# Performance work log

Hardware: AMD Instinct MI355X
Metric: run time of the kernel (lower is better)

The kernel has to match this reference:

```python
import jax, jax.numpy as jnp
import numpy as np

N_NODES = 100000
N_EDGES = 1600000
IN_CH = 128
HID = 128
OUT_CH = 16
N_GRAPHS = 64


def setup_inputs() -> dict:
    key = jax.random.key(0)
    ks = jax.random.split(key, 8)
    x = jax.random.normal(ks[0], (N_NODES, IN_CH), dtype=jnp.float32)
    edge_index = jax.random.randint(ks[1], (2, N_EDGES), 0, N_NODES, dtype=jnp.int64)
    batch = jnp.sort(jax.random.randint(ks[2], (N_NODES,), 0, N_GRAPHS, dtype=jnp.int64))
    s1 = 1.0 / np.sqrt(IN_CH)
    s2 = 1.0 / np.sqrt(HID)
    W1 = jax.random.uniform(ks[3], (IN_CH, HID), jnp.float32, -s1, s1)
    b1 = jnp.zeros((HID,), jnp.float32)
    W2 = jax.random.uniform(ks[4], (HID, HID), jnp.float32, -s2, s2)
    b2 = jnp.zeros((HID,), jnp.float32)
    Wfc = jax.random.uniform(ks[5], (HID, OUT_CH), jnp.float32, -s2, s2)
    bfc = jax.random.uniform(ks[6], (OUT_CH,), jnp.float32, -s2, s2)
    return {"x": x, "W1": W1, "b1": b1, "W2": W2, "b2": b2,
            "Wfc": Wfc, "bfc": bfc, "edge_index": edge_index, "batch": batch}


def _gcn_conv(x, W, b, src, dst, deg_inv_sqrt, deg_inv):
    # GCNConv with self-loops: out = D^-1/2 (A+I) D^-1/2 (x W) + b
    h = x @ W                                   # [N, H]
    norm = deg_inv_sqrt[src] * deg_inv_sqrt[dst]  # [E]
    agg = jax.ops.segment_sum(h[src] * norm[:, None], dst, num_segments=N_NODES)
    # self-loop term: deg_inv_sqrt[i]^2 * h[i]
    return agg + h * deg_inv[:, None] + b


def reference(x, W1, b1, W2, b2, Wfc, bfc, edge_index, batch):
    src, dst = edge_index[0], edge_index[1]
    # degree including self-loop
    deg = jax.ops.segment_sum(jnp.ones((N_EDGES,), jnp.float32), dst, num_segments=N_NODES) + 1.0
    deg_inv_sqrt = jax.lax.rsqrt(deg)
    deg_inv = 1.0 / deg
    h = jax.nn.relu(_gcn_conv(x, W1, b1, src, dst, deg_inv_sqrt, deg_inv))
    h = jax.nn.relu(_gcn_conv(h, W2, b2, src, dst, deg_inv_sqrt, deg_inv))
    # global mean pool over graphs
    sums = jax.ops.segment_sum(h, batch, num_segments=N_GRAPHS)          # [G, H]
    counts = jax.ops.segment_sum(jnp.ones((N_NODES,), jnp.float32), batch, num_segments=N_GRAPHS)
    pooled = sums / jnp.maximum(counts, 1.0)[:, None]
    return pooled @ Wfc + bfc
```

## Files before the change

kernel.cpp:

```cpp
#include <hip/hip_runtime.h>
#include <math.h>

#define NN 100000
#define NE 1600000
#define CH 128
#define OUTC 16
#define NG 64

#define CBSH 9
#define NCB 196
#define CHK 8192
#define MAXB 12288
#define PS 8

typedef __attribute__((ext_vector_type(8))) short bf16x8;
typedef __attribute__((ext_vector_type(4))) float f32x4;

__device__ __forceinline__ unsigned short f2bf(float f) {
    union { float f; unsigned u; } v; v.f = f;
    unsigned r = v.u + 0x7FFF + ((v.u >> 16) & 1);
    return (unsigned short)(r >> 16);
}
__device__ __forceinline__ float bflo(unsigned u) {
    union { unsigned u; float f; } v; v.u = u << 16; return v.f;
}
__device__ __forceinline__ float bfhi(unsigned u) {
    union { unsigned u; float f; } v; v.u = u & 0xffff0000u; return v.f;
}

__global__ void k_prep(const float* __restrict__ W1, const float* __restrict__ W2,
                       unsigned short* __restrict__ wt1, unsigned short* __restrict__ wt2,
                       const int* __restrict__ batch, int* __restrict__ gptr,
                       int* __restrict__ bcnt) {
    int i = blockIdx.x * 256 + threadIdx.x;
    if (i < CH * CH) {
        int k = i >> 7, n = i & 127;
        wt1[n * CH + k] = f2bf(W1[i]);
    } else if (i < 2 * CH * CH) {
        int j = i - CH * CH;
        int k = j >> 7, n = j & 127;
        wt2[n * CH + k] = f2bf(W2[j]);
    }
    if (i < NCB) bcnt[i] = 0;
    if (i < NN) {
        int b = batch[i];
        int prev = (i == 0) ? -1 : batch[i - 1];
        for (int g = prev + 1; g <= b; g++) gptr[g] = i;
        if (i == NN - 1) {
            for (int g = b + 1; g <= NG; g++) gptr[g] = NN;
        }
    }
}

__global__ __launch_bounds__(1024) void k_hist(const int* __restrict__ dst, int* __restrict__ bcnt) {
    __shared__ int h[NCB];
    int t = threadIdx.x;
    if (t < NCB) h[t] = 0;
    __syncthreads();
    int base = blockIdx.x * CHK;
#pragma unroll
    for (int i = 0; i < 8; i++) {
        int e = base + i * 1024 + t;
        if (e < NE) atomicAdd(&h[dst[e] >> CBSH], 1);
    }
    __syncthreads();
    if (t < NCB && h[t]) atomicAdd(&bcnt[t], h[t]);
}

__global__ __launch_bounds__(1024) void k_bscan(const int* __restrict__ bcnt, int* __restrict__ ebase,
                        int* __restrict__ gfill, float* __restrict__ pooled) {
    __shared__ int s[256];
    int t = threadIdx.x;
    if (t < 256) s[t] = (t < NCB) ? bcnt[t] : 0;
    __syncthreads();
    for (int off = 1; off < 256; off <<= 1) {
        int v = 0;
        if (t < 256 && t >= off) v = s[t - off];
        __syncthreads();
        if (t < 256) s[t] += v;
        __syncthreads();
    }
    if (t == 0) ebase[0] = 0;
    if (t < NCB) { ebase[t + 1] = s[t]; gfill[t] = 0; }
    for (int i = t; i < NG * CH; i += 1024) pooled[i] = 0.f;
}

__global__ __launch_bounds__(1024) void k_passA(const int* __restrict__ src, const int* __restrict__ dst,
                        const int* __restrict__ ebase, int* __restrict__ gfill,
                        unsigned* __restrict__ ebuf) {
    __shared__ unsigned lbuf[CHK];
    __shared__ unsigned char lbyte[CHK];
    __shared__ int hcnt[NCB];
    __shared__ int hbase[256];
    __shared__ int goff[NCB];
    int t = threadIdx.x;
    if (t < NCB) hcnt[t] = 0;
    __syncthreads();
    int base = blockIdx.x * CHK;
    int cb[8], slot[8]; unsigned pk[8];
#pragma unroll
    for (int i = 0; i < 8; i++) {
        int e = base + i * 1024 + t;
        cb[i] = -1;
        if (e < NE) {
            int d = dst[e], s = src[e];
            cb[i] = d >> CBSH;
            pk[i] = ((unsigned)s << CBSH) | (unsigned)(d & 511);
            slot[i] = atomicAdd(&hcnt[cb[i]], 1);
        }
    }
    __syncthreads();
    if (t < 256) hbase[t] = (t < NCB) ? hcnt[t] : 0;
    __syncthreads();
    for (int off = 1; off < 256; off <<= 1) {
        int v = 0;
        if (t < 256 && t >= off) v = hbase[t - off];
        __syncthreads();
        if (t < 256) hbase[t] += v;
        __syncthreads();
    }
    if (t < NCB) {
        int c = hcnt[t];
        int g = c ? atomicAdd(&gfill[t], c) : 0;
        goff[t] = ebase[t] + g - (hbase[t] - c);
    }
    __syncthreads();
#pragma unroll
    for (int i = 0; i < 8; i++) {
        if (cb[i] >= 0) {
            int pos = hbase[cb[i]] - hcnt[cb[i]] + slot[i];
            lbuf[pos] = pk[i];
            lbyte[pos] = (unsigned char)cb[i];
        }
    }
    __syncthreads();
    int total = min(NE - base, CHK);
    for (int p = t; p < total; p += 1024) {
        unsigned v = lbuf[p];
        int b = lbyte[p];
        ebuf[goff[b] + p] = v;
    }
}

__global__ __launch_bounds__(1024) void k_passB(const unsigned* __restrict__ ebuf, const int* __restrict__ ebase,
                        int* __restrict__ degi, int* __restrict__ rowst,
                        float* __restrict__ dis, int* __restrict__ csr) {
    __shared__ int cnt[512];
    __shared__ int nbase[512];
    __shared__ int fill[512];
    __shared__ int stage[MAXB];
    int t = threadIdx.x;
    int cb = blockIdx.x;
    int nb0 = cb << CBSH;
    int ncnt = min(512, NN - nb0);
    int e0 = ebase[cb], e1 = ebase[cb + 1];
    if (t < 512) { cnt[t] = 0; fill[t] = 0; }
    __syncthreads();
    for (int e = e0 + t; e < e1; e += 1024)
        atomicAdd(&cnt[ebuf[e] & 511], 1);
    __syncthreads();
    if (t < 512) nbase[t] = cnt[t];
    __syncthreads();
    for (int off = 1; off < 512; off <<= 1) {
        int v = 0;
        if (t < 512 && t >= off) v = nbase[t - off];
        __syncthreads();
        if (t < 512) nbase[t] += v;
        __syncthreads();
    }
    for (int e = e0 + t; e < e1; e += 1024) {
        unsigned v = ebuf[e];
        int local = v & 511;
        int s = atomicAdd(&fill[local], 1);
        stage[nbase[local] - cnt[local] + s] = (int)(v >> CBSH);
    }
    __syncthreads();
    int total = e1 - e0;
    for (int p = t; p < total; p += 1024) csr[e0 + p] = stage[p];
    if (t < ncnt) {
        int c = cnt[t];
        degi[nb0 + t] = c;
        rowst[nb0 + t] = e0 + nbase[t] - c;
        dis[nb0 + t] = rsqrtf((float)c + 1.0f);
    }
}

template<bool F32IN>
__launch_bounds__(256, 2)
__global__ void k_gemm(const void* __restrict__ Av,
                       const unsigned short* __restrict__ WT,
                       const float* __restrict__ dis,
                       unsigned short* __restrict__ out) {
    int tid = threadIdx.x;
    int wave = tid >> 6, lane = tid & 63;
    int quad = lane >> 4, l16 = lane & 15;

    int rbase = blockIdx.x * 128 + wave * 32;

    bf16x8 af[2][4];
#pragma unroll
    for (int s = 0; s < 2; s++) {
        int row = rbase + s * 16 + l16;
        if (row >= NN) row = NN - 1;
        if (F32IN) {
            const float* arow = (const float*)Av + (size_t)row * CH + quad * 8;
#pragma unroll
            for (int ks = 0; ks < 4; ks++) {
                float4 lo = *(const float4*)(arow + ks * 32);
                float4 hi = *(const float4*)(arow + ks * 32 + 4);
                union { bf16x8 v; unsigned short u[8]; } tmp;
                tmp.u[0] = f2bf(lo.x); tmp.u[1] = f2bf(lo.y);
                tmp.u[2] = f2bf(lo.z); tmp.u[3] = f2bf(lo.w);
                tmp.u[4] = f2bf(hi.x); tmp.u[5] = f2bf(hi.y);
                tmp.u[6] = f2bf(hi.z); tmp.u[7] = f2bf(hi.w);
                af[s][ks] = tmp.v;
            }
        } else {
            const unsigned short* arow = (const unsigned short*)Av + (size_t)row * CH + quad * 8;
#pragma unroll
            for (int ks = 0; ks < 4; ks++) af[s][ks] = *(const bf16x8*)(arow + ks * 32);
        }
    }

    f32x4 acc[2][8];
#pragma unroll
    for (int s = 0; s < 2; s++)
#pragma unroll
        for (int t = 0; t < 8; t++) acc[s][t] = (f32x4){0.f, 0.f, 0.f, 0.f};

#pragma unroll
    for (int t = 0; t < 8; t++) {
        const unsigned short* wcol = WT + (size_t)(t * 16 + l16) * CH + quad * 8;
        bf16x8 b0 = *(const bf16x8*)(wcol);
        bf16x8 b1 = *(const bf16x8*)(wcol + 32);
        bf16x8 b2 = *(const bf16x8*)(wcol + 64);
        bf16x8 b3 = *(const bf16x8*)(wcol + 96);
#pragma unroll
        for (int s = 0; s < 2; s++) {
            acc[s][t] = __builtin_amdgcn_mfma_f32_16x16x32_bf16(af[s][0], b0, acc[s][t], 0, 0, 0);
            acc[s][t] = __builtin_amdgcn_mfma_f32_16x16x32_bf16(af[s][1], b1, acc[s][t], 0, 0, 0);
            acc[s][t] = __builtin_amdgcn_mfma_f32_16x16x32_bf16(af[s][2], b2, acc[s][t], 0, 0, 0);
            acc[s][t] = __builtin_amdgcn_mfma_f32_16x16x32_bf16(af[s][3], b3, acc[s][t], 0, 0, 0);
        }
    }

#pragma unroll
    for (int s = 0; s < 2; s++) {
#pragma unroll
        for (int r = 0; r < 4; r++) {
            int orow = rbase + s * 16 + quad * 4 + r;
            if (orow < NN) {
                float d = dis[orow];
#pragma unroll
                for (int t = 0; t < 8; t++) {
                    out[(size_t)orow * CH + t * 16 + l16] = f2bf(acc[s][t][r] * d);
                }
            }
        }
    }
}

__global__ __launch_bounds__(256) void k_agg(const unsigned short* __restrict__ ht, const int* __restrict__ rowst,
                      const int* __restrict__ degi, const int* __restrict__ csr,
                      const float* __restrict__ dis, const float* __restrict__ bias,
                      unsigned short* __restrict__ out) {
    int t = threadIdx.x;
    int grp = t >> 4;
    int q = t & 15;
    int n = blockIdx.x * 16 + grp;
    const uint4* base = (const uint4*)ht;

    uint4 sv = base[(size_t)n * 16 + q];
    float a[8];
    a[0] = bflo(sv.x); a[1] = bfhi(sv.x);
    a[2] = bflo(sv.y); a[3] = bfhi(sv.y);
    a[4] = bflo(sv.z); a[5] = bfhi(sv.z);
    a[6] = bflo(sv.w); a[7] = bfhi(sv.w);

    int start = rowst[n];
    int c = degi[n];
    int nb = c & ~7;
    int j = 0;
    for (; j < nb; j += 8) {
        int idx[8];
#pragma unroll
        for (int u = 0; u < 8; u++) idx[u] = csr[start + j + u];
        uint4 v[8];
#pragma unroll
        for (int u = 0; u < 8; u++) v[u] = base[(size_t)idx[u] * 16 + q];
#pragma unroll
        for (int u = 0; u < 8; u++) {
            a[0] += bflo(v[u].x); a[1] += bfhi(v[u].x);
            a[2] += bflo(v[u].y); a[3] += bfhi(v[u].y);
            a[4] += bflo(v[u].z); a[5] += bfhi(v[u].z);
            a[6] += bflo(v[u].w); a[7] += bfhi(v[u].w);
        }
    }
    if (j < c) {
        int idx[8];
#pragma unroll
        for (int u = 0; u < 8; u++) { int e = j + u; idx[u] = csr[start + (e < c ? e : c - 1)]; }
        uint4 v[8];
#pragma unroll
        for (int u = 0; u < 8; u++) v[u] = base[(size_t)idx[u] * 16 + q];
#pragma unroll
        for (int u = 0; u < 8; u++) {
            if (j + u < c) {
                a[0] += bflo(v[u].x); a[1] += bfhi(v[u].x);
                a[2] += bflo(v[u].y); a[3] += bfhi(v[u].y);
                a[4] += bflo(v[u].z); a[5] += bfhi(v[u].z);
                a[6] += bflo(v[u].w); a[7] += bfhi(v[u].w);
            }
        }
    }

    float d = dis[n];
    const float4* bp = (const float4*)bias;
    float4 b0 = bp[q * 2], b1 = bp[q * 2 + 1];
    uint4 o;
    {
        float ox = fmaxf(fmaf(d, a[0], b0.x), 0.f), oy = fmaxf(fmaf(d, a[1], b0.y), 0.f);
        o.x = ((unsigned)f2bf(oy) << 16) | (unsigned)f2bf(ox);
        ox = fmaxf(fmaf(d, a[2], b0.z), 0.f); oy = fmaxf(fmaf(d, a[3], b0.w), 0.f);
        o.y = ((unsigned)f2bf(oy) << 16) | (unsigned)f2bf(ox);
        ox = fmaxf(fmaf(d, a[4], b1.x), 0.f); oy = fmaxf(fmaf(d, a[5], b1.y), 0.f);
        o.z = ((unsigned)f2bf(oy) << 16) | (unsigned)f2bf(ox);
        ox = fmaxf(fmaf(d, a[6], b1.z), 0.f); oy = fmaxf(fmaf(d, a[7], b1.w), 0.f);
        o.w = ((unsigned)f2bf(oy) << 16) | (unsigned)f2bf(ox);
    }
    ((uint4*)out)[(size_t)n * 16 + q] = o;
}

__global__ __launch_bounds__(512) void k_pool2(const unsigned short* __restrict__ h,
                                               const int* __restrict__ gptr,
                                               float* __restrict__ pooled) {
    int g = blockIdx.x >> 3;
    int s = blockIdx.x & 7;
    int gs = gptr[g], ge = gptr[g + 1];
    int len = ge - gs;
    int i0 = gs + (int)(((long long)len * s) >> 3);
    int i1 = gs + (int)(((long long)len * (s + 1)) >> 3);
    int t = threadIdx.x;
    int pr = t & 63;
    int ro = t >> 6;
    const unsigned* base = (const unsigned*)h;
    float s0 = 0.f, s1 = 0.f;
    for (int n = i0 + ro; n < i1; n += 8) {
        unsigned v = base[(size_t)n * 64 + pr];
        s0 += bflo(v); s1 += bfhi(v);
    }
    __shared__ float red[2][8][64];
    red[0][ro][pr] = s0; red[1][ro][pr] = s1;
    __syncthreads();
    for (int off = 4; off >= 1; off >>= 1) {
        if (ro < off) {
            red[0][ro][pr] += red[0][ro + off][pr];
            red[1][ro][pr] += red[1][ro + off][pr];
        }
        __syncthreads();
    }
    if (ro == 0) {
        atomicAdd(&pooled[g * CH + pr * 2],     red[0][0][pr]);
        atomicAdd(&pooled[g * CH + pr * 2 + 1], red[1][0][pr]);
    }
}

__global__ void k_final(const float* __restrict__ pooled, const int* __restrict__ gptr,
                        const float* __restrict__ Wfc, const float* __restrict__ bfc,
                        float* __restrict__ out) {
    int idx = blockIdx.x * 256 + threadIdx.x;
    if (idx >= NG * OUTC) return;
    int g = idx >> 4, o = idx & 15;
    float c = (float)(gptr[g + 1] - gptr[g]);
    float inv = 1.0f / fmaxf(c, 1.0f);
    float s = 0.f;
    for (int k = 0; k < CH; k++) s += pooled[g * CH + k] * Wfc[k * OUTC + o];
    out[idx] = fmaf(s, inv, bfc[o]);
}

extern "C" void kernel_launch(void* const* d_in, const int* in_sizes, int n_in,
                              void* d_out, int out_size, void* d_ws, size_t ws_size,
                              hipStream_t stream) {
    (void)in_sizes; (void)n_in; (void)out_size; (void)ws_size;
    const float* x   = (const float*)d_in[0];
    const float* W1  = (const float*)d_in[1];
    const float* b1  = (const float*)d_in[2];
    const float* W2  = (const float*)d_in[3];
    const float* b2  = (const float*)d_in[4];
    const float* Wfc = (const float*)d_in[5];
    const float* bfc = (const float*)d_in[6];
    const int* ei    = (const int*)d_in[7];
    const int* batch = (const int*)d_in[8];
    const int* esrc = ei;
    const int* edst = ei + NE;
    float* out = (float*)d_out;

    char* w = (char*)d_ws;
    unsigned short* bufA = (unsigned short*)w; w += (size_t)NN * CH * 2;
    unsigned short* bufB = (unsigned short*)w; w += (size_t)NN * CH * 2;
    unsigned short* wt1  = (unsigned short*)w; w += (size_t)CH * CH * 2;
    unsigned short* wt2  = (unsigned short*)w; w += (size_t)CH * CH * 2;
    unsigned* ebuf = (unsigned*)w; w += (size_t)NE * 4;
    int* csr    = (int*)w;    w += (size_t)NE * 4;
    int* degi   = (int*)w;    w += (size_t)NN * 4;
    int* rowst  = (int*)w;    w += (size_t)NN * 4;
    float* dis  = (float*)w;  w += (size_t)NN * 4;
    int* bcnt   = (int*)w;    w += NCB * 4;
    int* ebase  = (int*)w;    w += (NCB + 1) * 4;
    int* gfill  = (int*)w;    w += NCB * 4;
    int* gptr   = (int*)w;    w += (NG + 1) * 4;
    float* pooled = (float*)w; w += (size_t)NG * CH * 4;

    const int histBlocks = (NE + CHK - 1) / CHK;
    const int gemmBlocks = (NN + 127) / 128;
    const int aggBlocks  = NN / 16;

    k_prep<<<(NN + 255) / 256, 256, 0, stream>>>(W1, W2, wt1, wt2, batch, gptr, bcnt);
    k_hist<<<histBlocks, 1024, 0, stream>>>(edst, bcnt);
    k_bscan<<<1, 1024, 0, stream>>>(bcnt, ebase, gfill, pooled);
    k_passA<<<histBlocks, 1024, 0, stream>>>(esrc, edst, ebase, gfill, ebuf);
    k_passB<<<NCB, 1024, 0, stream>>>(ebuf, ebase, degi, rowst, dis, csr);

    k_gemm<true><<<gemmBlocks, 256, 0, stream>>>(x, wt1, dis, bufA);
    k_agg<<<aggBlocks, 256, 0, stream>>>(bufA, rowst, degi, csr, dis, b1, bufB);
    k_gemm<false><<<gemmBlocks, 256, 0, stream>>>(bufB, wt2, dis, bufA);
    k_agg<<<aggBlocks, 256, 0, stream>>>(bufA, rowst, degi, csr, dis, b2, bufB);

    k_pool2<<<NG * PS, 512, 0, stream>>>(bufB, gptr, pooled);
    k_final<<<(NG * OUTC + 255) / 256, 256, 0, stream>>>(pooled, gptr, Wfc, bfc, out);
}
```

Before: 319.2 us.

## Slice feature tables into 16-channel column blocks for cache-local neighbor gathers

Stores the hidden feature matrices as 8 column slices of 16 bf16 channels (slice-major), and splits aggregation so each block handles one slice for 128 nodes. Each slice table (~3.2MB) is meant to fit in cache, so random neighbor gathers hit L2/LLC instead of DRAM. Neighbor indices for the block are staged in LDS, and degree is derived from rowst[n+1] instead of a separate array. The cost is that every edge index is re-read once per slice (8x), and each gather fetches only 32 bytes, down from 256.

Measured after the change: 338.3 us. +6.0%, slower.

```diff
diff --git a/kernel.cpp b/kernel.cpp
--- a/kernel.cpp
+++ b/kernel.cpp
@@ -12,6 +12,8 @@
 #define CHK 8192
 #define MAXB 12288
 #define PS 8
+#define ANB 128
+#define ICAP 3072
 
 typedef __attribute__((ext_vector_type(8))) short bf16x8;
 typedef __attribute__((ext_vector_type(4))) float f32x4;
@@ -27,6 +29,7 @@
 __device__ __forceinline__ float bfhi(unsigned u) {
     union { unsigned u; float f; } v; v.u = u & 0xffff0000u; return v.f;
 }
+
 
 __global__ void k_prep(const float* __restrict__ W1, const float* __restrict__ W2,
                        unsigned short* __restrict__ wt1, unsigned short* __restrict__ wt2,
@@ -143,7 +146,7 @@
 }
 
 __global__ __launch_bounds__(1024) void k_passB(const unsigned* __restrict__ ebuf, const int* __restrict__ ebase,
-                        int* __restrict__ degi, int* __restrict__ rowst,
+                        int* __restrict__ rowst,
                         float* __restrict__ dis, int* __restrict__ csr) {
     __shared__ int cnt[512];
     __shared__ int nbase[512];
@@ -179,10 +182,10 @@
     for (int p = t; p < total; p += 1024) csr[e0 + p] = stage[p];
     if (t < ncnt) {
         int c = cnt[t];
-        degi[nb0 + t] = c;
         rowst[nb0 + t] = e0 + nbase[t] - c;
         dis[nb0 + t] = rsqrtf((float)c + 1.0f);
     }
+    if (cb == NCB - 1 && t == 0) rowst[NN] = e1;
 }
 
 template<bool F32IN>
@@ -216,9 +219,13 @@
                 af[s][ks] = tmp.v;
             }
         } else {
-            const unsigned short* arow = (const unsigned short*)Av + (size_t)row * CH + quad * 8;
-#pragma unroll
-            for (int ks = 0; ks < 4; ks++) af[s][ks] = *(const bf16x8*)(arow + ks * 32);
+            const unsigned short* A = (const unsigned short*)Av;
+#pragma unroll
+            for (int ks = 0; ks < 4; ks++) {
+                int c = ks * 32 + quad * 8;
+                const unsigned short* p = A + ((size_t)(c >> 4) * NN + row) * 16 + (c & 15);
+                af[s][ks] = *(const bf16x8*)p;
+            }
         }
     }
 
@@ -253,72 +260,91 @@
                 float d = dis[orow];
 #pragma unroll
                 for (int t = 0; t < 8; t++) {
-                    out[(size_t)orow * CH + t * 16 + l16] = f2bf(acc[s][t][r] * d);
+                    out[((size_t)t * NN + orow) * 16 + l16] = f2bf(acc[s][t][r] * d);
                 }
             }
         }
     }
 }
 
-__global__ __launch_bounds__(256) void k_agg(const unsigned short* __restrict__ ht, const int* __restrict__ rowst,
-                      const int* __restrict__ degi, const int* __restrict__ csr,
-                      const float* __restrict__ dis, const float* __restrict__ bias,
+__global__ __launch_bounds__(256) void k_agg(const unsigned short* __restrict__ ht,
+                      const int* __restrict__ rowst,
+                      const float* __restrict__ dis, const int* __restrict__ csr,
+                      const float* __restrict__ bias,
                       unsigned short* __restrict__ out) {
-    int t = threadIdx.x;
-    int grp = t >> 4;
-    int q = t & 15;
-    int n = blockIdx.x * 16 + grp;
-    const uint4* base = (const uint4*)ht;
-
-    uint4 sv = base[(size_t)n * 16 + q];
-    float a[8];
-    a[0] = bflo(sv.x); a[1] = bfhi(sv.x);
-    a[2] = bflo(sv.y); a[3] = bfhi(sv.y);
-    a[4] = bflo(sv.z); a[5] = bfhi(sv.z);
-    a[6] = bflo(sv.w); a[7] = bfhi(sv.w);
-
-    int start = rowst[n];
-    int c = degi[n];
-    int nb = c & ~7;
-    int j = 0;
-    for (; j < nb; j += 8) {
-        int idx[8];
-#pragma unroll
-        for (int u = 0; u < 8; u++) idx[u] = csr[start + j + u];
-        uint4 v[8];
-#pragma unroll
-        for (int u = 0; u < 8; u++) v[u] = base[(size_t)idx[u] * 16 + q];
-#pragma unroll
-        for (int u = 0; u < 8; u++) {
-            a[0] += bflo(v[u].x); a[1] += bfhi(v[u].x);
-            a[2] += bflo(v[u].y); a[3] += bfhi(v[u].y);
-            a[4] += bflo(v[u].z); a[5] += bfhi(v[u].z);
-            a[6] += bflo(v[u].w); a[7] += bfhi(v[u].w);
-        }
-    }
-    if (j < c) {
-        int idx[8];
-#pragma unroll
-        for (int u = 0; u < 8; u++) { int e = j + u; idx[u] = csr[start + (e < c ? e : c - 1)]; }
-        uint4 v[8];
-#pragma unroll
-        for (int u = 0; u < 8; u++) v[u] = base[(size_t)idx[u] * 16 + q];
-#pragma unroll
-        for (int u = 0; u < 8; u++) {
-            if (j + u < c) {
-                a[0] += bflo(v[u].x); a[1] += bfhi(v[u].x);
-                a[2] += bflo(v[u].y); a[3] += bfhi(v[u].y);
-                a[4] += bflo(v[u].z); a[5] += bfhi(v[u].z);
-                a[6] += bflo(v[u].w); a[7] += bfhi(v[u].w);
+    __shared__ int sidx[ICAP];
+    int t = threadIdx.x;
+    int sl = blockIdx.x & 7;
+    int g0 = (blockIdx.x >> 3) * ANB;
+    int p = t & 1;
+    int n = g0 + (t >> 1);
+    const uint4* tab = (const uint4*)(ht + (size_t)sl * NN * 16);
+
+    int start = 0, c = 0; float d = 0.f; uint4 sv = (uint4){0u,0u,0u,0u};
+    if (n < NN) {
+        start = rowst[n];
+        c = rowst[n + 1] - start;
+        d = dis[n];
+        sv = tab[(size_t)n * 2 + p];
+    }
+
+    int nlast = min(g0 + ANB - 1, NN - 1);
+    int s0 = rowst[g0];
+    int len = rowst[nlast + 1] - s0;
+    bool fast = (len <= ICAP);
+    if (fast) {
+        for (int i = t; i < len; i += 256) sidx[i] = csr[s0 + i];
+    }
+    __syncthreads();
+
+    if (n < NN) {
+        float a[8];
+        a[0] = bflo(sv.x); a[1] = bfhi(sv.x);
+        a[2] = bflo(sv.y); a[3] = bfhi(sv.y);
+        a[4] = bflo(sv.z); a[5] = bfhi(sv.z);
+        a[6] = bflo(sv.w); a[7] = bfhi(sv.w);
+
+        int off = start - s0;
+        if (fast) {
+            for (int j = 0; j < c; j += 8) {
+                int idx[8];
+#pragma unroll
+                for (int u = 0; u < 8; u++) { int e = j + u; idx[u] = sidx[off + (e < c ? e : c - 1)]; }
+                uint4 v[8];
+#pragma unroll
+                for (int u = 0; u < 8; u++) v[u] = tab[(size_t)idx[u] * 2 + p];
+#pragma unroll
+                for (int u = 0; u < 8; u++) {
+                    if (j + u >= c) v[u] = (uint4){0u, 0u, 0u, 0u};
+                    a[0] += bflo(v[u].x); a[1] += bfhi(v[u].x);
+                    a[2] += bflo(v[u].y); a[3] += bfhi(v[u].y);
+                    a[4] += bflo(v[u].z); a[5] += bfhi(v[u].z);
+                    a[6] += bflo(v[u].w); a[7] += bfhi(v[u].w);
+                }
             }
-        }
-    }
-
-    float d = dis[n];
-    const float4* bp = (const float4*)bias;
-    float4 b0 = bp[q * 2], b1 = bp[q * 2 + 1];
-    uint4 o;
-    {
+        } else {
+            for (int j = 0; j < c; j += 8) {
+                int idx[8];
+#pragma unroll
+                for (int u = 0; u < 8; u++) { int e = j + u; idx[u] = csr[start + (e < c ? e : c - 1)]; }
+                uint4 v[8];
+#pragma unroll
+                for (int u = 0; u < 8; u++) v[u] = tab[(size_t)idx[u] * 2 + p];
+#pragma unroll
+                for (int u = 0; u < 8; u++) {
+                    if (j + u >= c) v[u] = (uint4){0u, 0u, 0u, 0u};
+                    a[0] += bflo(v[u].x); a[1] += bfhi(v[u].x);
+                    a[2] += bflo(v[u].y); a[3] += bfhi(v[u].y);
+                    a[4] += bflo(v[u].z); a[5] += bfhi(v[u].z);
+                    a[6] += bflo(v[u].w); a[7] += bfhi(v[u].w);
+                }
+            }
+        }
+
+        const float* bb = bias + sl * 16 + p * 8;
+        float4 b0 = *(const float4*)bb;
+        float4 b1 = *(const float4*)(bb + 4);
+        uint4 o;
         float ox = fmaxf(fmaf(d, a[0], b0.x), 0.f), oy = fmaxf(fmaf(d, a[1], b0.y), 0.f);
         o.x = ((unsigned)f2bf(oy) << 16) | (unsigned)f2bf(ox);
         ox = fmaxf(fmaf(d, a[2], b0.z), 0.f); oy = fmaxf(fmaf(d, a[3], b0.w), 0.f);
@@ -327,8 +353,8 @@
         o.z = ((unsigned)f2bf(oy) << 16) | (unsigned)f2bf(ox);
         ox = fmaxf(fmaf(d, a[6], b1.z), 0.f); oy = fmaxf(fmaf(d, a[7], b1.w), 0.f);
         o.w = ((unsigned)f2bf(oy) << 16) | (unsigned)f2bf(ox);
-    }
-    ((uint4*)out)[(size_t)n * 16 + q] = o;
+        ((uint4*)out)[((size_t)sl * NN + n) * 2 + p] = o;
+    }
 }
 
 __global__ __launch_bounds__(512) void k_pool2(const unsigned short* __restrict__ h,
@@ -343,10 +369,11 @@
     int t = threadIdx.x;
     int pr = t & 63;
     int ro = t >> 6;
+    int sl = pr >> 3, wd = pr & 7;
     const unsigned* base = (const unsigned*)h;
     float s0 = 0.f, s1 = 0.f;
     for (int n = i0 + ro; n < i1; n += 8) {
-        unsigned v = base[(size_t)n * 64 + pr];
+        unsigned v = base[((size_t)sl * NN + n) * 8 + wd];
         s0 += bflo(v); s1 += bfhi(v);
     }
     __shared__ float red[2][8][64];
@@ -402,8 +429,7 @@
     unsigned short* wt2  = (unsigned short*)w; w += (size_t)CH * CH * 2;
     unsigned* ebuf = (unsigned*)w; w += (size_t)NE * 4;
     int* csr    = (int*)w;    w += (size_t)NE * 4;
-    int* degi   = (int*)w;    w += (size_t)NN * 4;
-    int* rowst  = (int*)w;    w += (size_t)NN * 4;
+    int* rowst  = (int*)w;    w += (size_t)(NN + 1) * 4;
     float* dis  = (float*)w;  w += (size_t)NN * 4;
     int* bcnt   = (int*)w;    w += NCB * 4;
     int* ebase  = (int*)w;    w += (NCB + 1) * 4;
@@ -413,18 +439,18 @@
 
     const int histBlocks = (NE + CHK - 1) / CHK;
     const int gemmBlocks = (NN + 127) / 128;
-    const int aggBlocks  = NN / 16;
+    const int aggBlocks  = ((NN + ANB - 1) / ANB) * 8;
 
     k_prep<<<(NN + 255) / 256, 256, 0, stream>>>(W1, W2, wt1, wt2, batch, gptr, bcnt);
     k_hist<<<histBlocks, 1024, 0, stream>>>(edst, bcnt);
     k_bscan<<<1, 1024, 0, stream>>>(bcnt, ebase, gfill, pooled);
     k_passA<<<histBlocks, 1024, 0, stream>>>(esrc, edst, ebase, gfill, ebuf);
-    k_passB<<<NCB, 1024, 0, stream>>>(ebuf, ebase, degi, rowst, dis, csr);
+    k_passB<<<NCB, 1024, 0, stream>>>(ebuf, ebase, rowst, dis, csr);
 
     k_gemm<true><<<gemmBlocks, 256, 0, stream>>>(x, wt1, dis, bufA);
-    k_agg<<<aggBlocks, 256, 0, stream>>>(bufA, rowst, degi, csr, dis, b1, bufB);
+    k_agg<<<aggBlocks, 256, 0, stream>>>(bufA, rowst, dis, csr, b1, bufB);
     k_gemm<false><<<gemmBlocks, 256, 0, stream>>>(bufB, wt2, dis, bufA);
-    k_agg<<<aggBlocks, 256, 0, stream>>>(bufA, rowst, degi, csr, dis, b2, bufB);
+    k_agg<<<aggBlocks, 256, 0, stream>>>(bufA, rowst, dis, csr, b2, bufB);
 
     k_pool2<<<NG * PS, 512, 0, stream>>>(bufB, gptr, pooled);
     k_final<<<(NG * OUTC + 255) / 256, 256, 0, stream>>>(pooled, gptr, Wfc, bfc, out);
```

## Fold bucket scan into consumers, fuse pool with final FC, vectorize GEMM stores

Applied to the files above, without the earlier changes.

Removes the single-block bucket-scan kernel: passA and passB each recompute the prefix sum of bucket counts in shared memory, and the zeroing of gfill and pooled moves into k_prep. The pooling kernel now also does the final FC, using a done counter so the last block to finish computes the output, which removes one more launch. The GEMM swaps its MFMA operands so each lane holds four consecutive columns of one row and writes them as a packed 8-byte store instead of scattered 2-byte stores. Together this saves two kernel launches at the cost of redundant scans in every block and a serialized final FC in one block.

New measurement: 332.9 us. 4.3% more time.

```diff
diff --git a/kernel.cpp b/kernel.cpp
--- a/kernel.cpp
+++ b/kernel.cpp
@@ -31,7 +31,8 @@
 __global__ void k_prep(const float* __restrict__ W1, const float* __restrict__ W2,
                        unsigned short* __restrict__ wt1, unsigned short* __restrict__ wt2,
                        const int* __restrict__ batch, int* __restrict__ gptr,
-                       int* __restrict__ bcnt) {
+                       int* __restrict__ bcnt, int* __restrict__ gfill,
+                       float* __restrict__ pooled, int* __restrict__ done) {
     int i = blockIdx.x * 256 + threadIdx.x;
     if (i < CH * CH) {
         int k = i >> 7, n = i & 127;
@@ -41,7 +42,9 @@
         int k = j >> 7, n = j & 127;
         wt2[n * CH + k] = f2bf(W2[j]);
     }
-    if (i < NCB) bcnt[i] = 0;
+    if (i < NCB) { bcnt[i] = 0; gfill[i] = 0; }
+    if (i < NG * CH) pooled[i] = 0.f;
+    if (i == 0) *done = 0;
     if (i < NN) {
         int b = batch[i];
         int prev = (i == 0) ? -1 : batch[i - 1];
@@ -67,34 +70,18 @@
     if (t < NCB && h[t]) atomicAdd(&bcnt[t], h[t]);
 }
 
-__global__ __launch_bounds__(1024) void k_bscan(const int* __restrict__ bcnt, int* __restrict__ ebase,
-                        int* __restrict__ gfill, float* __restrict__ pooled) {
-    __shared__ int s[256];
-    int t = threadIdx.x;
-    if (t < 256) s[t] = (t < NCB) ? bcnt[t] : 0;
-    __syncthreads();
-    for (int off = 1; off < 256; off <<= 1) {
-        int v = 0;
-        if (t < 256 && t >= off) v = s[t - off];
-        __syncthreads();
-        if (t < 256) s[t] += v;
-        __syncthreads();
-    }
-    if (t == 0) ebase[0] = 0;
-    if (t < NCB) { ebase[t + 1] = s[t]; gfill[t] = 0; }
-    for (int i = t; i < NG * CH; i += 1024) pooled[i] = 0.f;
-}
-
 __global__ __launch_bounds__(1024) void k_passA(const int* __restrict__ src, const int* __restrict__ dst,
-                        const int* __restrict__ ebase, int* __restrict__ gfill,
+                        const int* __restrict__ bcnt, int* __restrict__ gfill,
                         unsigned* __restrict__ ebuf) {
     __shared__ unsigned lbuf[CHK];
     __shared__ unsigned char lbyte[CHK];
     __shared__ int hcnt[NCB];
     __shared__ int hbase[256];
+    __shared__ int eb[256];
     __shared__ int goff[NCB];
     int t = threadIdx.x;
     if (t < NCB) hcnt[t] = 0;
+    if (t < 256) eb[t] = (t < NCB) ? bcnt[t] : 0;
     __syncthreads();
     int base = blockIdx.x * CHK;
     int cb[8], slot[8]; unsigned pk[8];
@@ -113,16 +100,17 @@
     if (t < 256) hbase[t] = (t < NCB) ? hcnt[t] : 0;
     __syncthreads();
     for (int off = 1; off < 256; off <<= 1) {
-        int v = 0;
-        if (t < 256 && t >= off) v = hbase[t - off];
-        __syncthreads();
-        if (t < 256) hbase[t] += v;
+        int v1 = 0, v2 = 0;
+        if (t < 256 && t >= off) { v1 = hbase[t - off]; v2 = eb[t - off]; }
+        __syncthreads();
+        if (t < 256 && t >= off) { hbase[t] += v1; eb[t] += v2; }
         __syncthreads();
     }
     if (t < NCB) {
         int c = hcnt[t];
         int g = c ? atomicAdd(&gfill[t], c) : 0;
-        goff[t] = ebase[t] + g - (hbase[t] - c);
+        int ebase_t = t ? eb[t - 1] : 0;
+        goff[t] = ebase_t + g - (hbase[t] - c);
     }
     __syncthreads();
 #pragma unroll
@@ -142,20 +130,30 @@
     }
 }
 
-__global__ __launch_bounds__(1024) void k_passB(const unsigned* __restrict__ ebuf, const int* __restrict__ ebase,
+__global__ __launch_bounds__(1024) void k_passB(const unsigned* __restrict__ ebuf, const int* __restrict__ bcnt,
                         int* __restrict__ degi, int* __restrict__ rowst,
                         float* __restrict__ dis, int* __restrict__ csr) {
     __shared__ int cnt[512];
     __shared__ int nbase[512];
     __shared__ int fill[512];
     __shared__ int stage[MAXB];
+    __shared__ int eb[256];
     int t = threadIdx.x;
     int cb = blockIdx.x;
     int nb0 = cb << CBSH;
     int ncnt = min(512, NN - nb0);
-    int e0 = ebase[cb], e1 = ebase[cb + 1];
     if (t < 512) { cnt[t] = 0; fill[t] = 0; }
-    __syncthreads();
+    if (t < 256) eb[t] = (t < NCB) ? bcnt[t] : 0;
+    __syncthreads();
+    for (int off = 1; off < 256; off <<= 1) {
+        int v = 0;
+        if (t < 256 && t >= off) v = eb[t - off];
+        __syncthreads();
+        if (t < 256 && t >= off) eb[t] += v;
+        __syncthreads();
+    }
+    int e0 = cb ? eb[cb - 1] : 0;
+    int e1 = eb[cb];
     for (int e = e0 + t; e < e1; e += 1024)
         atomicAdd(&cnt[ebuf[e] & 511], 1);
     __syncthreads();
@@ -237,24 +235,25 @@
         bf16x8 b3 = *(const bf16x8*)(wcol + 96);
 #pragma unroll
         for (int s = 0; s < 2; s++) {
-            acc[s][t] = __builtin_amdgcn_mfma_f32_16x16x32_bf16(af[s][0], b0, acc[s][t], 0, 0, 0);
-            acc[s][t] = __builtin_amdgcn_mfma_f32_16x16x32_bf16(af[s][1], b1, acc[s][t], 0, 0, 0);
-            acc[s][t] = __builtin_amdgcn_mfma_f32_16x16x32_bf16(af[s][2], b2, acc[s][t], 0, 0, 0);
-            acc[s][t] = __builtin_amdgcn_mfma_f32_16x16x32_bf16(af[s][3], b3, acc[s][t], 0, 0, 0);
+            acc[s][t] = __builtin_amdgcn_mfma_f32_16x16x32_bf16(b0, af[s][0], acc[s][t], 0, 0, 0);
+            acc[s][t] = __builtin_amdgcn_mfma_f32_16x16x32_bf16(b1, af[s][1], acc[s][t], 0, 0, 0);
+            acc[s][t] = __builtin_amdgcn_mfma_f32_16x16x32_bf16(b2, af[s][2], acc[s][t], 0, 0, 0);
+            acc[s][t] = __builtin_amdgcn_mfma_f32_16x16x32_bf16(b3, af[s][3], acc[s][t], 0, 0, 0);
         }
     }
 
 #pragma unroll
     for (int s = 0; s < 2; s++) {
-#pragma unroll
-        for (int r = 0; r < 4; r++) {
-            int orow = rbase + s * 16 + quad * 4 + r;
-            if (orow < NN) {
-                float d = dis[orow];
-#pragma unroll
-                for (int t = 0; t < 8; t++) {
-                    out[(size_t)orow * CH + t * 16 + l16] = f2bf(acc[s][t][r] * d);
-                }
+        int node = rbase + s * 16 + l16;
+        int cl = (node < NN) ? node : NN - 1;
+        float d = dis[cl];
+        if (node < NN) {
+#pragma unroll
+            for (int t = 0; t < 8; t++) {
+                unsigned lo = ((unsigned)f2bf(acc[s][t][1] * d) << 16) | (unsigned)f2bf(acc[s][t][0] * d);
+                unsigned hi = ((unsigned)f2bf(acc[s][t][3] * d) << 16) | (unsigned)f2bf(acc[s][t][2] * d);
+                uint2 pk; pk.x = lo; pk.y = hi;
+                *(uint2*)(out + (size_t)node * CH + t * 16 + quad * 4) = pk;
             }
         }
     }
@@ -331,9 +330,13 @@
     ((uint4*)out)[(size_t)n * 16 + q] = o;
 }
 
-__global__ __launch_bounds__(512) void k_pool2(const unsigned short* __restrict__ h,
+__global__ __launch_bounds__(512) void k_pool_final(const unsigned short* __restrict__ h,
                                                const int* __restrict__ gptr,
-                                               float* __restrict__ pooled) {
+                                               float* __restrict__ pooled,
+                                               int* __restrict__ done,
+                                               const float* __restrict__ Wfc,
+                                               const float* __restrict__ bfc,
+                                               float* __restrict__ out) {
     int g = blockIdx.x >> 3;
     int s = blockIdx.x & 7;
     int gs = gptr[g], ge = gptr[g + 1];
@@ -363,19 +366,27 @@
         atomicAdd(&pooled[g * CH + pr * 2],     red[0][0][pr]);
         atomicAdd(&pooled[g * CH + pr * 2 + 1], red[1][0][pr]);
     }
-}
-
-__global__ void k_final(const float* __restrict__ pooled, const int* __restrict__ gptr,
-                        const float* __restrict__ Wfc, const float* __restrict__ bfc,
-                        float* __restrict__ out) {
-    int idx = blockIdx.x * 256 + threadIdx.x;
-    if (idx >= NG * OUTC) return;
-    int g = idx >> 4, o = idx & 15;
-    float c = (float)(gptr[g + 1] - gptr[g]);
-    float inv = 1.0f / fmaxf(c, 1.0f);
-    float s = 0.f;
-    for (int k = 0; k < CH; k++) s += pooled[g * CH + k] * Wfc[k * OUTC + o];
-    out[idx] = fmaf(s, inv, bfc[o]);
+
+    __shared__ int lastFlag;
+    __shared__ float plds[NG * CH];
+    __syncthreads();
+    if (t == 0) {
+        __threadfence();
+        int r = atomicAdd(done, 1);
+        lastFlag = (r == NG * PS - 1) ? 1 : 0;
+    }
+    __syncthreads();
+    if (!lastFlag) return;
+    for (int i = t; i < NG * CH; i += 512) plds[i] = atomicAdd(&pooled[i], 0.0f);
+    __syncthreads();
+    for (int idx = t; idx < NG * OUTC; idx += 512) {
+        int gg = idx >> 4, o = idx & 15;
+        float c = (float)(gptr[gg + 1] - gptr[gg]);
+        float inv = 1.0f / fmaxf(c, 1.0f);
+        float acc = 0.f;
+        for (int k = 0; k < CH; k++) acc += plds[gg * CH + k] * Wfc[k * OUTC + o];
+        out[idx] = fmaf(acc, inv, bfc[o]);
+    }
 }
 
 extern "C" void kernel_launch(void* const* d_in, const int* in_sizes, int n_in,
@@ -406,26 +417,24 @@
     int* rowst  = (int*)w;    w += (size_t)NN * 4;
     float* dis  = (float*)w;  w += (size_t)NN * 4;
     int* bcnt   = (int*)w;    w += NCB * 4;
-    int* ebase  = (int*)w;    w += (NCB + 1) * 4;
     int* gfill  = (int*)w;    w += NCB * 4;
     int* gptr   = (int*)w;    w += (NG + 1) * 4;
     float* pooled = (float*)w; w += (size_t)NG * CH * 4;
+    int* done   = (int*)w;    w += 4;
 
     const int histBlocks = (NE + CHK - 1) / CHK;
     const int gemmBlocks = (NN + 127) / 128;
     const int aggBlocks  = NN / 16;
 
-    k_prep<<<(NN + 255) / 256, 256, 0, stream>>>(W1, W2, wt1, wt2, batch, gptr, bcnt);
+    k_prep<<<(NN + 255) / 256, 256, 0, stream>>>(W1, W2, wt1, wt2, batch, gptr, bcnt, gfill, pooled, done);
     k_hist<<<histBlocks, 1024, 0, stream>>>(edst, bcnt);
-    k_bscan<<<1, 1024, 0, stream>>>(bcnt, ebase, gfill, pooled);
-    k_passA<<<histBlocks, 1024, 0, stream>>>(esrc, edst, ebase, gfill, ebuf);
-    k_passB<<<NCB, 1024, 0, stream>>>(ebuf, ebase, degi, rowst, dis, csr);
+    k_passA<<<histBlocks, 1024, 0, stream>>>(esrc, edst, bcnt, gfill, ebuf);
+    k_passB<<<NCB, 1024, 0, stream>>>(ebuf, bcnt, degi, rowst, dis, csr);
 
     k_gemm<true><<<gemmBlocks, 256, 0, stream>>>(x, wt1, dis, bufA);
     k_agg<<<aggBlocks, 256, 0, stream>>>(bufA, rowst, degi, csr, dis, b1, bufB);
     k_gemm<false><<<gemmBlocks, 256, 0, stream>>>(bufB, wt2, dis, bufA);
     k_agg<<<aggBlocks, 256, 0, stream>>>(bufA, rowst, degi, csr, dis, b2, bufB);
 
-    k_pool2<<<NG * PS, 512, 0, stream>>>(bufB, gptr, pooled);
-    k_final<<<(NG * OUTC + 255) / 256, 256, 0, stream>>>(pooled, gptr, Wfc, bfc, out);
-}
+    k_pool_final<<<NG * PS, 512, 0, stream>>>(bufB, gptr, pooled, done, Wfc, bfc, out);
+}
```
